# Kernel optimization log

Hardware: AMD Instinct MI355X
Metric: run time of the kernel (lower is better)

Reference implementation:

```python
import jax, jax.numpy as jnp
import numpy as np

KEEP_RATIO = 0.5
TEMPERATURE = 1.0
MIN_GATE = 0.0
EPS = 1e-06


def setup_inputs() -> dict:
    key = jax.random.key(0)
    k1, k2 = jax.random.split(key)
    B, C = 8192, 4096
    token = jax.random.normal(k1, (B, C), dtype=jnp.float32)
    proxy = jax.random.normal(k2, (B, C), dtype=jnp.float32)
    return {"token": token, "proxy": proxy}


def reference(token, proxy):
    tok = token  # [B, C]
    px = jax.lax.stop_gradient(proxy)  # detach_proxy=True
    score = jnp.abs(tok * px)  # [B, C]
    B, C = score.shape
    k = max(1, int(round(C * KEEP_RATIO)))
    # hard mask: top-k indices per row -> scatter 1.0
    _, topk_idx = jax.lax.top_k(score, k)  # [B, k]
    rows = jnp.arange(B)[:, None]
    hard_mask = jnp.zeros_like(score).at[rows, topk_idx].set(1.0)
    # per-row standardization (torch.std is unbiased -> ddof=1)
    mu = jnp.mean(score, axis=-1, keepdims=True)
    sigma = jnp.maximum(jnp.std(score, axis=-1, ddof=1, keepdims=True), EPS)
    z = (score - mu) / sigma / max(TEMPERATURE, EPS)
    soft_gate = jax.nn.sigmoid(z)
    if MIN_GATE > 0:
        soft_gate = soft_gate * (1.0 - MIN_GATE) + MIN_GATE
    gate = soft_gate * (1.0 - hard_mask) + hard_mask
    return tok * gate
```

## Files before the change

### kernel.cpp

```cpp
#include <hip/hip_runtime.h>
#include <math.h>

#define CLS   4096
#define KSEL  2048u
#define TPB   256

typedef float f32x4 __attribute__((ext_vector_type(4)));


template<int SHIFT, int NBITS, int BPL>
__device__ __forceinline__ void radix_small(const float sc[16], unsigned* hist,
        int lane, unsigned& prefix, unsigned& kr, unsigned& cnt_eq)
{
    const unsigned msk = (1u << NBITS) - 1u;
    #pragma unroll
    for (int i = 0; i < 16; ++i) {
        unsigned u = __float_as_uint(sc[i]);
        if ((u >> (SHIFT + NBITS)) == (prefix >> (SHIFT + NBITS)))
            atomicAdd(&hist[(u >> SHIFT) & msk], 1u);
    }
    __syncthreads();
    unsigned c[BPL];
    if constexpr (BPL == 4) {
        uint4 x = *(const uint4*)&hist[lane * 4];
        c[0] = x.x; c[1] = x.y; c[2] = x.z; c[3] = x.w;
    } else {
        c[0] = hist[lane];
    }
    unsigned sfx[BPL + 1]; sfx[BPL] = 0;
    #pragma unroll
    for (int j = BPL - 1; j >= 0; --j) sfx[j] = sfx[j + 1] + c[j];
    const unsigned tot = sfx[0];
    unsigned s = tot;
    #pragma unroll
    for (int off = 1; off < 64; off <<= 1) {
        unsigned t = __shfl_down(s, off);
        if (lane + off < 64) s += t;
    }
    const unsigned Sx = s - tot;
    const bool has = (Sx < kr) && (kr <= Sx + tot);
    unsigned bin = 0, below = 0, ceq = 0;
    if (has) {
        #pragma unroll
        for (int j = 0; j < BPL; ++j)
            if (Sx + sfx[j] >= kr && Sx + sfx[j + 1] < kr) {
                bin = (unsigned)(lane * BPL + j);
                below = Sx + sfx[j + 1];
                ceq = c[j];
            }
    }
    unsigned long long m = __ballot(has);
    int src = (int)__builtin_ctzll(m);
    bin = __shfl(bin, src); below = __shfl(below, src); ceq = __shfl(ceq, src);
    prefix |= bin << SHIFT;
    kr -= below;
    cnt_eq = ceq;
}

__global__ __launch_bounds__(TPB) void proxy_gate_kernel(
    const float* __restrict__ token,
    const float* __restrict__ proxy,
    float* __restrict__ out)
{
    __shared__ __align__(16) unsigned char lds[18816];
    unsigned* h0   = (unsigned*)(lds);
    unsigned* h1   = (unsigned*)(lds + 16416);
    unsigned* h2   = (unsigned*)(lds + 17456);
    unsigned* h3   = (unsigned*)(lds + 18496);
    unsigned* s_wt = (unsigned*)(lds + 18752);
    unsigned* s_bc = (unsigned*)(lds + 18768);
    float*    s_fr = (float*)   (lds + 18784);
    unsigned char* s_flag = lds;
    unsigned*      s_suf  = (unsigned*)(lds + 8192);

    const int tid  = threadIdx.x;
    const int lane = tid & 63;
    const int wv   = tid >> 6;
    const size_t base = (size_t)blockIdx.x * CLS;
    const float4* t4 = (const float4*)(token + base);
    const float4* p4 = (const float4*)(proxy + base);
    f32x4* o4 = (f32x4*)(out + base);

    float4 tv[4], pv[4];
    #pragma unroll
    for (int i = 0; i < 4; ++i) { tv[i] = t4[i*TPB + tid]; pv[i] = p4[i*TPB + tid]; }
    {
        uint4 z = make_uint4(0u, 0u, 0u, 0u);
        uint4* zp = (uint4*)lds;
        #pragma unroll
        for (int m = 0; m < 5; ++m) { int idx = m*TPB + tid; if (idx < 1172) zp[idx] = z; }
    }

    float tok[16], sc[16];
    float sum = 0.f, sumsq = 0.f;
    #pragma unroll
    for (int i = 0; i < 4; ++i) {
        float a;
        a = fabsf(tv[i].x*pv[i].x); tok[i*4+0]=tv[i].x; sc[i*4+0]=a; sum+=a; sumsq+=a*a;
        a = fabsf(tv[i].y*pv[i].y); tok[i*4+1]=tv[i].y; sc[i*4+1]=a; sum+=a; sumsq+=a*a;
        a = fabsf(tv[i].z*pv[i].z); tok[i*4+2]=tv[i].z; sc[i*4+2]=a; sum+=a; sumsq+=a*a;
        a = fabsf(tv[i].w*pv[i].w); tok[i*4+3]=tv[i].w; sc[i*4+3]=a; sum+=a; sumsq+=a*a;
    }
    __syncthreads();

    {
        unsigned* h0c = h0 + (((tid >> 2) & 1) ? 2052 : 0);
        #pragma unroll
        for (int i = 0; i < 16; ++i)
            atomicAdd(&h0c[__float_as_uint(sc[i]) >> 20], 1u);
    }
    #pragma unroll
    for (int off = 32; off > 0; off >>= 1) {
        sum   += __shfl_xor(sum, off);
        sumsq += __shfl_xor(sumsq, off);
    }
    if (lane == 0) { s_fr[wv] = sum; s_fr[4+wv] = sumsq; }
    __syncthreads();

    const float tot_s = s_fr[0]+s_fr[1]+s_fr[2]+s_fr[3];
    const float tot_q = s_fr[4]+s_fr[5]+s_fr[6]+s_fr[7];
    const float mu = tot_s * (1.0f/CLS);
    float var = (tot_q - tot_s*mu) * (1.0f/(CLS-1));
    var = fmaxf(var, 0.0f);
    const float inv_sigma = 1.0f / fmaxf(sqrtf(var), 1e-6f);

    unsigned kr = KSEL, prefix = 0, cnt_eq = 0;
    {
        const int bo = tid * 8;
        uint4 x0 = *(const uint4*)&h0[bo];
        uint4 x1 = *(const uint4*)&h0[bo + 4];
        uint4 y0 = *(const uint4*)&h0[2052 + bo];
        uint4 y1 = *(const uint4*)&h0[2052 + bo + 4];
        unsigned c[8] = { x0.x+y0.x, x0.y+y0.y, x0.z+y0.z, x0.w+y0.w,
                          x1.x+y1.x, x1.y+y1.y, x1.z+y1.z, x1.w+y1.w };
        unsigned sfx[9]; sfx[8] = 0;
        #pragma unroll
        for (int j = 7; j >= 0; --j) sfx[j] = sfx[j+1] + c[j];
        const unsigned tot = sfx[0];
        unsigned s = tot;
        #pragma unroll
        for (int off = 1; off < 64; off <<= 1) {
            unsigned t = __shfl_down(s, off);
            if (lane + off < 64) s += t;
        }
        if (lane == 0) s_wt[wv] = s;
        __syncthreads();
        unsigned addhi = 0;
        #pragma unroll
        for (int w2 = 0; w2 < 4; ++w2) if (w2 > wv) addhi += s_wt[w2];
        const unsigned Sx = (s - tot) + addhi;
        if (Sx < kr && kr <= Sx + tot) {
            #pragma unroll
            for (int j = 0; j < 8; ++j)
                if (Sx + sfx[j] >= kr && Sx + sfx[j+1] < kr) {
                    s_bc[0] = (unsigned)(bo + j);
                    s_bc[1] = Sx + sfx[j+1];
                    s_bc[2] = c[j];
                }
        }
        __syncthreads();
        prefix = s_bc[0] << 20;
        kr    -= s_bc[1];
        cnt_eq = s_bc[2];
    }

    radix_small<12, 8, 4>(sc, h1, lane, prefix, kr, cnt_eq);
    radix_small< 4, 8, 4>(sc, h2, lane, prefix, kr, cnt_eq);
    radix_small< 0, 4, 1>(sc, h3, lane, prefix, kr, cnt_eq);

    const float thr = __uint_as_float(prefix);
    const bool tie_rare = (cnt_eq != kr);

    if (tie_rare) {
        #pragma unroll
        for (int i = 0; i < 4; ++i) {
            #pragma unroll
            for (int c2 = 0; c2 < 4; ++c2)
                s_flag[i*1024 + tid*4 + c2] = (sc[i*4+c2] == thr) ? 1 : 0;
        }
        __syncthreads();
        unsigned lc = 0;
        unsigned char mf[16];
        #pragma unroll
        for (int m = 0; m < 16; ++m) { mf[m] = s_flag[tid*16 + m]; lc += mf[m]; }
        s_suf[tid] = lc;
        __syncthreads();
        #pragma unroll
        for (int off = 1; off < 256; off <<= 1) {
            unsigned w = s_suf[tid] + ((tid >= off) ? s_suf[tid - off] : 0u);
            __syncthreads();
            s_suf[tid] = w;
            __syncthreads();
        }
        unsigned r = s_suf[tid] - lc;
        #pragma unroll
        for (int m = 0; m < 16; ++m) {
            if (mf[m]) { s_flag[tid*16 + m] = (r < kr) ? 2 : 0; ++r; }
        }
        __syncthreads();
    }

    #pragma unroll
    for (int i = 0; i < 4; ++i) {
        float res[4];
        #pragma unroll
        for (int c2 = 0; c2 < 4; ++c2) {
            const float s = sc[i*4+c2];
            const float z = (s - mu) * inv_sigma;
            const float soft = 1.0f / (1.0f + __expf(-z));
            bool hard;
            if (tie_rare)
                hard = (s > thr) || ((s == thr) && (s_flag[i*1024 + tid*4 + c2] == 2));
            else
                hard = (s >= thr);
            res[c2] = tok[i*4+c2] * (hard ? 1.0f : soft);
        }
        f32x4 rv = { res[0], res[1], res[2], res[3] };
        __builtin_nontemporal_store(rv, &o4[i*TPB + tid]);
    }
}

extern "C" void kernel_launch(void* const* d_in, const int* in_sizes, int n_in,
                              void* d_out, int out_size, void* d_ws, size_t ws_size,
                              hipStream_t stream) {
    const float* token = (const float*)d_in[0];
    const float* proxy = (const float*)d_in[1];
    float* outp = (float*)d_out;
    const int B = in_sizes[0] / CLS;
    hipLaunchKernelGGL(proxy_gate_kernel, dim3(B), dim3(TPB), 0, stream,
                       token, proxy, outp);
}
```

Before: 70.32 us.

## Replace later radix passes with candidate compaction and wave ballot bit-select

After the first 12-bit histogram pass, elements that fall in the threshold bin are compacted into LDS with packed low bits and index. When there are at most 256 of them, one wave finds the exact k-th key with a 32-step ballot bit search, which replaces three histogram passes and the tie-break scan. The first histogram also gets a swizzled slot layout to cut LDS bank conflicts. This adds a ballot-heavy compaction step and keeps the old radix path as a fallback for large candidate counts.

```diff
diff --git a/kernel.cpp b/kernel.cpp
--- a/kernel.cpp
+++ b/kernel.cpp
@@ -7,6 +7,11 @@
 
 typedef float f32x4 __attribute__((ext_vector_type(4)));
 
+
+__device__ __forceinline__ int h0slot(unsigned b) {
+    unsigned j = b & 7u, t = b >> 3;
+    return (int)((j << 8) | ((t + 4u*j) & 255u));
+}
 
 template<int SHIFT, int NBITS, int BPL>
 __device__ __forceinline__ void radix_small(const float sc[16], unsigned* hist,
@@ -57,19 +62,57 @@
     cnt_eq = ceq;
 }
 
+template<int K>
+__device__ __forceinline__ unsigned ballot_sel(const unsigned* cand, unsigned cnt,
+                                               unsigned kr, int lane)
+{
+    unsigned key[K]; unsigned long long m[K];
+    #pragma unroll
+    for (int w = 0; w < K; ++w) {
+        unsigned base = (unsigned)w * 64u;
+        bool v = (base + (unsigned)lane) < cnt;
+        key[w] = v ? cand[base + lane] : 0u;
+        unsigned rem = (cnt > base) ? (cnt - base) : 0u;
+        m[w] = (rem >= 64u) ? ~0ull : ((rem == 0u) ? 0ull : ((1ull << rem) - 1ull));
+    }
+    unsigned Kstar = 0u;
+    #pragma unroll
+    for (int b = 31; b >= 0; --b) {
+        unsigned long long t[K];
+        unsigned c1 = 0;
+        #pragma unroll
+        for (int w = 0; w < K; ++w) {
+            t[w] = m[w] & __ballot((key[w] >> b) & 1u);
+            c1 += (unsigned)__popcll(t[w]);
+        }
+        if (c1 >= kr) {
+            #pragma unroll
+            for (int w = 0; w < K; ++w) m[w] = t[w];
+            Kstar |= (1u << b);
+        } else {
+            kr -= c1;
+            #pragma unroll
+            for (int w = 0; w < K; ++w) m[w] &= ~t[w];
+        }
+    }
+    return Kstar;
+}
+
 __global__ __launch_bounds__(TPB) void proxy_gate_kernel(
     const float* __restrict__ token,
     const float* __restrict__ proxy,
     float* __restrict__ out)
 {
     __shared__ __align__(16) unsigned char lds[18816];
-    unsigned* h0   = (unsigned*)(lds);
-    unsigned* h1   = (unsigned*)(lds + 16416);
-    unsigned* h2   = (unsigned*)(lds + 17456);
-    unsigned* h3   = (unsigned*)(lds + 18496);
-    unsigned* s_wt = (unsigned*)(lds + 18752);
-    unsigned* s_bc = (unsigned*)(lds + 18768);
-    float*    s_fr = (float*)   (lds + 18784);
+    unsigned* h0    = (unsigned*)(lds);
+    unsigned* cand  = (unsigned*)(lds + 16416);
+    unsigned* h1    = (unsigned*)(lds + 16416);
+    unsigned* h2    = (unsigned*)(lds + 17456);
+    unsigned* h3    = (unsigned*)(lds + 18496);
+    unsigned* s_cnt = (unsigned*)(lds + 18752);
+    unsigned* s_wt  = (unsigned*)(lds + 18756);
+    unsigned* s_bc  = (unsigned*)(lds + 18772);
+    float*    s_fr  = (float*)   (lds + 18784);
     unsigned char* s_flag = lds;
     unsigned*      s_suf  = (unsigned*)(lds + 8192);
 
@@ -88,7 +131,8 @@
         uint4 z = make_uint4(0u, 0u, 0u, 0u);
         uint4* zp = (uint4*)lds;
         #pragma unroll
-        for (int m = 0; m < 5; ++m) { int idx = m*TPB + tid; if (idx < 1172) zp[idx] = z; }
+        for (int m = 0; m < 5; ++m) { int idx = m*TPB + tid; if (idx < 1026) zp[idx] = z; }
+        if (tid == 0) *s_cnt = 0u;
     }
 
     float tok[16], sc[16];
@@ -107,7 +151,7 @@
         unsigned* h0c = h0 + (((tid >> 2) & 1) ? 2052 : 0);
         #pragma unroll
         for (int i = 0; i < 16; ++i)
-            atomicAdd(&h0c[__float_as_uint(sc[i]) >> 20], 1u);
+            atomicAdd(&h0c[h0slot(__float_as_uint(sc[i]) >> 20)], 1u);
     }
     #pragma unroll
     for (int off = 32; off > 0; off >>= 1) {
@@ -124,15 +168,14 @@
     var = fmaxf(var, 0.0f);
     const float inv_sigma = 1.0f / fmaxf(sqrtf(var), 1e-6f);
 
-    unsigned kr = KSEL, prefix = 0, cnt_eq = 0;
+    unsigned kr = KSEL, cnt_eq = 0;
     {
-        const int bo = tid * 8;
-        uint4 x0 = *(const uint4*)&h0[bo];
-        uint4 x1 = *(const uint4*)&h0[bo + 4];
-        uint4 y0 = *(const uint4*)&h0[2052 + bo];
-        uint4 y1 = *(const uint4*)&h0[2052 + bo + 4];
-        unsigned c[8] = { x0.x+y0.x, x0.y+y0.y, x0.z+y0.z, x0.w+y0.w,
-                          x1.x+y1.x, x1.y+y1.y, x1.z+y1.z, x1.w+y1.w };
+        unsigned c[8];
+        #pragma unroll
+        for (int j = 0; j < 8; ++j) {
+            int sl = (j << 8) | ((tid + 4*j) & 255);
+            c[j] = h0[sl] + h0[2052 + sl];
+        }
         unsigned sfx[9]; sfx[8] = 0;
         #pragma unroll
         for (int j = 7; j >= 0; --j) sfx[j] = sfx[j+1] + c[j];
@@ -153,51 +196,89 @@
             #pragma unroll
             for (int j = 0; j < 8; ++j)
                 if (Sx + sfx[j] >= kr && Sx + sfx[j+1] < kr) {
-                    s_bc[0] = (unsigned)(bo + j);
+                    s_bc[0] = (unsigned)(tid*8 + j);
                     s_bc[1] = Sx + sfx[j+1];
                     s_bc[2] = c[j];
                 }
         }
         __syncthreads();
-        prefix = s_bc[0] << 20;
         kr    -= s_bc[1];
         cnt_eq = s_bc[2];
     }
-
-    radix_small<12, 8, 4>(sc, h1, lane, prefix, kr, cnt_eq);
-    radix_small< 4, 8, 4>(sc, h2, lane, prefix, kr, cnt_eq);
-    radix_small< 0, 4, 1>(sc, h3, lane, prefix, kr, cnt_eq);
-
-    const float thr = __uint_as_float(prefix);
-    const bool tie_rare = (cnt_eq != kr);
-
-    if (tie_rare) {
-        #pragma unroll
-        for (int i = 0; i < 4; ++i) {
-            #pragma unroll
-            for (int c2 = 0; c2 < 4; ++c2)
-                s_flag[i*1024 + tid*4 + c2] = (sc[i*4+c2] == thr) ? 1 : 0;
+    const unsigned bin = s_bc[0];
+
+    {
+        unsigned wtot = 0;
+        #pragma unroll
+        for (int ii = 0; ii < 16; ++ii) {
+            bool cnd = ((__float_as_uint(sc[ii]) >> 20) == bin);
+            wtot += (unsigned)__popcll(__ballot(cnd));
+        }
+        unsigned wbase = 0;
+        if (lane == 0) wbase = atomicAdd(s_cnt, wtot);
+        wbase = __shfl(wbase, 0);
+        unsigned run = wbase;
+        #pragma unroll
+        for (int ii = 0; ii < 16; ++ii) {
+            unsigned u = __float_as_uint(sc[ii]);
+            bool cnd = ((u >> 20) == bin);
+            unsigned long long mm = __ballot(cnd);
+            if (cnd) {
+                unsigned pos = run + (unsigned)__popcll(mm & ((1ull << lane) - 1ull));
+                unsigned idx = (unsigned)((ii >> 2)*1024 + tid*4 + (ii & 3));
+                if (pos < 256u) cand[pos] = ((u & 0xFFFFFu) << 12) | (4095u - idx);
+            }
+            run += (unsigned)__popcll(mm);
+        }
+    }
+    __syncthreads();
+    const unsigned cnt = *s_cnt;
+    const bool ballot_mode = (cnt <= 256u);
+
+    unsigned Kstar = 0;
+    float thr = 0.f; bool tie_rare = false; unsigned prefix = bin << 20;
+    if (ballot_mode) {
+        Kstar = (cnt <= 128u) ? ballot_sel<2>(cand, cnt, kr, lane)
+                              : ballot_sel<4>(cand, cnt, kr, lane);
+    } else {
+        {
+            unsigned* hz = (unsigned*)(lds + 16416);
+            #pragma unroll
+            for (int m = 0; m < 3; ++m) { int ix = m*TPB + tid; if (ix < 584) hz[ix] = 0u; }
         }
         __syncthreads();
-        unsigned lc = 0;
-        unsigned char mf[16];
-        #pragma unroll
-        for (int m = 0; m < 16; ++m) { mf[m] = s_flag[tid*16 + m]; lc += mf[m]; }
-        s_suf[tid] = lc;
-        __syncthreads();
-        #pragma unroll
-        for (int off = 1; off < 256; off <<= 1) {
-            unsigned w = s_suf[tid] + ((tid >= off) ? s_suf[tid - off] : 0u);
+        radix_small<12, 8, 4>(sc, h1, lane, prefix, kr, cnt_eq);
+        radix_small< 4, 8, 4>(sc, h2, lane, prefix, kr, cnt_eq);
+        radix_small< 0, 4, 1>(sc, h3, lane, prefix, kr, cnt_eq);
+        thr = __uint_as_float(prefix);
+        tie_rare = (cnt_eq != kr);
+        if (tie_rare) {
+            #pragma unroll
+            for (int i = 0; i < 4; ++i)
+                #pragma unroll
+                for (int c2 = 0; c2 < 4; ++c2)
+                    s_flag[i*1024 + tid*4 + c2] = (sc[i*4+c2] == thr) ? 1 : 0;
             __syncthreads();
-            s_suf[tid] = w;
+            unsigned lc = 0;
+            unsigned char mf[16];
+            #pragma unroll
+            for (int m = 0; m < 16; ++m) { mf[m] = s_flag[tid*16 + m]; lc += mf[m]; }
+            s_suf[tid] = lc;
             __syncthreads();
-        }
-        unsigned r = s_suf[tid] - lc;
-        #pragma unroll
-        for (int m = 0; m < 16; ++m) {
-            if (mf[m]) { s_flag[tid*16 + m] = (r < kr) ? 2 : 0; ++r; }
-        }
-        __syncthreads();
+            #pragma unroll
+            for (int off = 1; off < 256; off <<= 1) {
+                unsigned w = s_suf[tid] + ((tid >= off) ? s_suf[tid - off] : 0u);
+                __syncthreads();
+                s_suf[tid] = w;
+                __syncthreads();
+            }
+            unsigned r = s_suf[tid] - lc;
+            #pragma unroll
+            for (int m = 0; m < 16; ++m) {
+                if (mf[m]) { s_flag[tid*16 + m] = (r < kr) ? 2 : 0; ++r; }
+            }
+            __syncthreads();
+        }
     }
 
     #pragma unroll
@@ -209,10 +290,17 @@
             const float z = (s - mu) * inv_sigma;
             const float soft = 1.0f / (1.0f + __expf(-z));
             bool hard;
-            if (tie_rare)
+            const unsigned u = __float_as_uint(s);
+            if (ballot_mode) {
+                const unsigned e = u >> 20;
+                const unsigned idx = (unsigned)(i*1024 + tid*4 + c2);
+                const unsigned packed = ((u & 0xFFFFFu) << 12) | (4095u - idx);
+                hard = (e > bin) || ((e == bin) && (packed >= Kstar));
+            } else if (tie_rare) {
                 hard = (s > thr) || ((s == thr) && (s_flag[i*1024 + tid*4 + c2] == 2));
-            else
+            } else {
                 hard = (s >= thr);
+            }
             res[c2] = tok[i*4+c2] * (hard ? 1.0f : soft);
         }
         f32x4 rv = { res[0], res[1], res[2], res[3] };
```

Result: slower. 75.52 us (+7.4%).
